# Kernel optimization log

Hardware: AMD Instinct MI355X
Metric: run time of the kernel (lower is better)

The kernel has to match this reference:

```python
import jax, jax.numpy as jnp
import numpy as np

NR, NL, K, TOPK, C, B = 4096, 16384, 8, 10, 16, 4
W_OCC, W_MDN, W_INT = 0.2, 1.0, 0.1
LOG2PI = float(np.log(2.0 * np.pi))


def setup_inputs() -> dict:
    key = jax.random.key(0)
    ks = jax.random.split(key, 12)
    radar_indices = jnp.concatenate([
        jax.random.randint(ks[0], (NR, 1), 0, B),
        jax.random.randint(ks[1], (NR, 1), 0, 41),
        jax.random.randint(ks[2], (NR, 2), 0, 176),
    ], axis=1).astype(jnp.int32)
    lidar_indices = jnp.concatenate([
        jax.random.randint(ks[3], (NL, 1), 0, B),
        jax.random.randint(ks[4], (NL, 1), 0, 41),
        jax.random.randint(ks[5], (NL, 2), 0, 176),
    ], axis=1).astype(jnp.int32)
    return {
        'mu_off': jax.random.normal(ks[6], (NR, K, 3)) * 2.0,
        'log_sig_off': jax.random.normal(ks[7], (NR, K, 3)) * 0.3,
        'mu_int': jax.random.normal(ks[8], (NR, K, 1)),
        'occ_logit': jax.random.normal(ks[9], (NR, K, 1)),
        'mix_logit': jax.random.normal(ks[10], (NR, K, 1)),
        'lidar_features': jax.random.normal(ks[11], (NL, C)),
        'radar_indices': radar_indices,
        'lidar_indices': lidar_indices,
        'gt_topk': TOPK,
    }


def _match(radar_indices, lidar_indices, topk):
    # per-batch top-k nearest lidar voxels for each radar voxel (vectorized:
    # dense masked distance matrix replaces the per-batch python loop)
    rb, lb = radar_indices[:, 0], lidar_indices[:, 0]
    rpos = radar_indices[:, 1:].astype(jnp.float32)  # (Nr,3) zyx
    lpos = lidar_indices[:, 1:].astype(jnp.float32)  # (Nl,3)
    d2 = ((rpos * rpos).sum(-1)[:, None] + (lpos * lpos).sum(-1)[None, :]
          - 2.0 * (rpos @ lpos.T))  # (Nr,Nl) squared dist, same order as cdist
    same = rb[:, None] == lb[None, :]
    d2 = jnp.where(same, d2, jnp.inf)  # cross-batch pairs excluded
    _, nn_idx = jax.lax.top_k(-d2, topk)  # (Nr,topk) smallest distances
    matched = same.any(axis=1)  # (Nr,)
    offs_zyx = (lidar_indices[nn_idx, 1:]
                - radar_indices[:, None, 1:]).astype(jnp.float32)  # (Nr,topk,3)
    offs_zyx = jnp.where(matched[:, None, None], offs_zyx, 0.0)
    return matched, nn_idx, offs_zyx


def reference(mu_off, log_sig_off, mu_int, occ_logit, mix_logit,
              lidar_features, radar_indices, lidar_indices, gt_topk):
    matched, nn_idx, offs_zyx = _match(radar_indices, lidar_indices, gt_topk)
    gt_feat = jnp.where(matched[:, None, None], lidar_features[nn_idx], 0.0)  # (Nr,T,C)
    y = offs_zyx[..., ::-1]  # flip zyx -> xyz, (Nr,T,3)

    # occupancy BCE-with-logits against matched mask
    occ_any = occ_logit[..., 0].max(axis=1)  # (Nr,)
    tgt = matched.astype(occ_any.dtype)
    occ_loss = (tgt * jax.nn.softplus(-occ_any)
                + (1.0 - tgt) * jax.nn.softplus(occ_any)).mean()

    # MDN log-prob: (Nr,T,K) mixture components
    log_pi = jax.nn.log_softmax(mix_logit[..., 0], axis=1)  # (Nr,K)
    mu_ = mu_off[:, None, :, :]       # (Nr,1,K,3)
    ls_ = log_sig_off[:, None, :, :]
    sigma2 = jnp.exp(2.0 * ls_) + 1e-12
    y_ = y[:, :, None, :]             # (Nr,T,1,3)
    logN = -0.5 * (((y_ - mu_) ** 2) / sigma2 + 2.0 * ls_ + LOG2PI).sum(-1)  # (Nr,T,K)
    log_post = logN + log_pi[:, None, :]
    logp = jax.nn.logsumexp(log_post, axis=-1)  # (Nr,T)

    # masked means emulate boolean-index-then-mean over matched rows
    m = matched.astype(jnp.float32)
    cnt = m.sum()
    T = logp.shape[1]
    mdn_nll = -(logp * m[:, None]).sum() / (cnt * T)

    # intensity loss (C % 4 == 0 path)
    gt_int = gt_feat.reshape(gt_feat.shape[0], gt_feat.shape[1], C // 4, 4)[..., 3].mean(axis=2)  # (Nr,T)
    r = jax.nn.softmax(log_post, axis=-1)  # (Nr,T,K) responsibilities
    term = r * jnp.abs(mu_int[:, None, :, 0] - gt_int[:, :, None])  # (Nr,T,K)
    int_loss = (term * m[:, None, None]).sum() / (cnt * T * r.shape[-1])

    return W_OCC * occ_loss + W_MDN * mdn_nll + W_INT * int_loss
```

## Files before the change

kernel.cpp:

```cpp
#include <hip/hip_runtime.h>
#include <cstdint>

#define NRAD 4096
#define NLID 16384
#define KMIX 8
#define TOPK 10
#define CF   16
#define LOG2PI 1.8378770664093453f
#define MAIN_BLOCKS 1024

static constexpr unsigned INF_D2 = 62851u;

__device__ __forceinline__ void insert_key(unsigned (&t)[TOPK], unsigned key) {
#pragma unroll
    for (int i = TOPK - 1; i >= 1; --i) {
        unsigned hi = key > t[i - 1] ? key : t[i - 1];
        t[i] = hi < t[i] ? hi : t[i];
    }
    t[0] = key < t[0] ? key : t[0];
}

__device__ __forceinline__ void merge10(unsigned (&t)[TOPK], int lane,
                                        unsigned& mine, unsigned& first, unsigned& tenth) {
#pragma unroll
    for (int r = 0; r < TOPK; ++r) {
        unsigned v = t[0];
#pragma unroll
        for (int off = 32; off >= 1; off >>= 1) {
            unsigned o = __shfl_xor(v, off, 64);
            v = o < v ? o : v;
        }
        if (t[0] == v) {
#pragma unroll
            for (int i = 0; i < TOPK - 1; ++i) t[i] = t[i + 1];
            t[TOPK - 1] = 0xFFFFFFFFu;
        }
        if (lane == r) mine = v;
        if (r == 0) first = v;
        if (r == TOPK - 1) tenth = v;
    }
}

__device__ __forceinline__ float waveReduceSum(float v) {
#pragma unroll
    for (int off = 32; off >= 1; off >>= 1) v += __shfl_down(v, off, 64);
    return v;
}

__global__ __launch_bounds__(256) void prep_kernel(
        const int* __restrict__ lidar_indices,
        unsigned* __restrict__ packed_full,
        uint2* __restrict__ compacted,
        int* __restrict__ cursor) {
    int i = blockIdx.x * 256 + threadIdx.x;
    int lane = threadIdx.x & 63;
    int4 li = ((const int4*)lidar_indices)[i];
    int b = li.x;
    unsigned pos = ((unsigned)li.y << 16) | ((unsigned)li.z << 8) | (unsigned)li.w;
    packed_full[i] = ((unsigned)b << 22) | pos;
#pragma unroll
    for (int b2 = 0; b2 < 4; ++b2) {
        unsigned long long mask = __ballot(b == b2);
        if (b == b2) {
            int leader = __ffsll(mask) - 1;
            int off = (int)__popcll(mask & ((1ull << lane) - 1ull));
            int s = 0;
            if (lane == leader) s = atomicAdd(&cursor[b2], (int)__popcll(mask));
            s = __shfl(s, leader, 64);
            compacted[b2 * NLID + s + off] = make_uint2(pos, (unsigned)i);
        }
    }
}

__global__ __launch_bounds__(256) void main_kernel(
        const float* __restrict__ mu_off, const float* __restrict__ log_sig_off,
        const float* __restrict__ mu_int, const float* __restrict__ occ_logit,
        const float* __restrict__ mix_logit, const float* __restrict__ lidar_features,
        const int* __restrict__ radar_indices, const int* __restrict__ lidar_indices,
        const uint2* __restrict__ compacted, const unsigned* __restrict__ packed_full,
        const int* __restrict__ cursor, float4* __restrict__ partials,
        unsigned* __restrict__ dctr, float* __restrict__ out) {
    int tid = threadIdx.x, lane = tid & 63, wid = tid >> 6;
    int row = blockIdx.x * 4 + wid;

    int4 ri = ((const int4*)radar_indices)[row];
    int rb = ri.x, rz = ri.y, ry = ri.z, rx = ri.w;
    int c_cnt = cursor[rb];

    unsigned t[TOPK];
#pragma unroll
    for (int i = 0; i < TOPK; ++i) t[i] = 0xFFFFFFFFu;

    const uint4* src = (const uint4*)(compacted + rb * NLID);
    int iters = (c_cnt + 127) >> 7;
    uint4 q0 = src[lane];
    uint4 q1 = src[64 + lane];
    for (int it = 0; it < iters; ++it) {
        uint4 qn = src[(it + 2) * 64 + lane];
        int c0 = (it * 64 + lane) * 2;
        {
            int dz = (int)((q0.x >> 16) & 63u)  - rz;
            int dy = (int)((q0.x >> 8)  & 255u) - ry;
            int dx = (int)(q0.x & 255u)         - rx;
            unsigned d2 = (unsigned)(dz * dz + dy * dy + dx * dx);
            unsigned key = (c0 < c_cnt) ? ((d2 << 14) | q0.y) : 0xFFFFFFFFu;
            if (key < t[TOPK - 1]) insert_key(t, key);
        }
        {
            int dz = (int)((q0.z >> 16) & 63u)  - rz;
            int dy = (int)((q0.z >> 8)  & 255u) - ry;
            int dx = (int)(q0.z & 255u)         - rx;
            unsigned d2 = (unsigned)(dz * dz + dy * dy + dx * dx);
            unsigned key = (c0 + 1 < c_cnt) ? ((d2 << 14) | q0.w) : 0xFFFFFFFFu;
            if (key < t[TOPK - 1]) insert_key(t, key);
        }
        q0 = q1; q1 = qn;
    }

    unsigned mine = 0, first = 0, tenth = 0;
    merge10(t, lane, mine, first, tenth);
    bool matched = true;

    if (tenth == 0xFFFFFFFFu) {
#pragma unroll
        for (int i = 0; i < TOPK; ++i) t[i] = 0xFFFFFFFFu;
        for (int it = 0; it < NLID / 256; ++it) {
            uint4 p4 = ((const uint4*)packed_full)[it * 64 + lane];
            unsigned base = it * 256 + lane * 4;
            unsigned ps[4] = {p4.x, p4.y, p4.z, p4.w};
#pragma unroll
            for (int j = 0; j < 4; ++j) {
                unsigned p = ps[j];
                int b  = (int)(p >> 22);
                int dz = (int)((p >> 16) & 63u)  - rz;
                int dy = (int)((p >> 8)  & 255u) - ry;
                int dx = (int)(p & 255u)         - rx;
                unsigned d2 = (unsigned)(dz * dz + dy * dy + dx * dx);
                unsigned hi = (b == rb) ? d2 : INF_D2;
                insert_key(t, (hi << 14) | (base + j));
            }
        }
        merge10(t, lane, mine, first, tenth);
        matched = first < (INF_D2 << 14);
    }

    float mf = matched ? 1.f : 0.f;
    float lp = 0.f, ip = 0.f, oc = 0.f, mc = 0.f;
    if (lane < TOPK) {
        int nni = (int)(mine & 0x3FFFu);
        int4 ll = ((const int4*)lidar_indices)[nni];
        float y0 = mf * (float)(ll.w - rx);
        float y1 = mf * (float)(ll.z - ry);
        float y2 = mf * (float)(ll.y - rz);

        float mix[KMIX];
        float mmax = -1e30f;
#pragma unroll
        for (int k = 0; k < KMIX; ++k) {
            mix[k] = mix_logit[row * KMIX + k];
            mmax = fmaxf(mmax, mix[k]);
        }
        float msum = 0.f;
#pragma unroll
        for (int k = 0; k < KMIX; ++k) msum += __expf(mix[k] - mmax);
        float logZ = mmax + __logf(msum);

        float lpost[KMIX];
        float pmax = -1e30f;
#pragma unroll
        for (int k = 0; k < KMIX; ++k) {
            int bidx = (row * KMIX + k) * 3;
            float mu0 = mu_off[bidx + 0], mu1 = mu_off[bidx + 1], mu2 = mu_off[bidx + 2];
            float l0 = log_sig_off[bidx + 0], l1 = log_sig_off[bidx + 1], l2 = log_sig_off[bidx + 2];
            float s0 = __expf(2.f * l0) + 1e-12f;
            float s1 = __expf(2.f * l1) + 1e-12f;
            float s2 = __expf(2.f * l2) + 1e-12f;
            float d0 = y0 - mu0, d1 = y1 - mu1, d2v = y2 - mu2;
            float qq = d0 * d0 / s0 + d1 * d1 / s1 + d2v * d2v / s2
                     + 2.f * (l0 + l1 + l2) + 3.f * LOG2PI;
            lpost[k] = -0.5f * qq + (mix[k] - logZ);
            pmax = fmaxf(pmax, lpost[k]);
        }
        float ex[KMIX];
        float se = 0.f;
#pragma unroll
        for (int k = 0; k < KMIX; ++k) { ex[k] = __expf(lpost[k] - pmax); se += ex[k]; }
        float logp = pmax + __logf(se);

        float gt = 0.f;
        if (matched) {
            const float* lf = lidar_features + nni * CF;
            gt = 0.25f * (lf[3] + lf[7] + lf[11] + lf[15]);
        }
        float inv_se = 1.f / se;
        float isum = 0.f;
#pragma unroll
        for (int k = 0; k < KMIX; ++k)
            isum += ex[k] * inv_se * fabsf(mu_int[row * KMIX + k] - gt);

        lp = mf * logp;
        ip = mf * isum;
        if (lane == 0) {
            float oa = -1e30f;
#pragma unroll
            for (int k = 0; k < KMIX; ++k) oa = fmaxf(oa, occ_logit[row * KMIX + k]);
            float soft_abs = log1pf(__expf(-fabsf(oa)));
            oc = mf * (soft_abs + fmaxf(-oa, 0.f)) + (1.f - mf) * (soft_abs + fmaxf(oa, 0.f));
            mc = mf;
        }
    }

    lp = waveReduceSum(lp); ip = waveReduceSum(ip);
    oc = waveReduceSum(oc); mc = waveReduceSum(mc);
    __shared__ float sA[4], sB[4], sC[4], sD[4];
    __shared__ int isLast;
    if (lane == 0) { sA[wid] = lp; sB[wid] = ip; sC[wid] = oc; sD[wid] = mc; }
    __syncthreads();
    if (tid == 0) {
        partials[blockIdx.x] = make_float4(sA[0] + sA[1] + sA[2] + sA[3],
                                           sB[0] + sB[1] + sB[2] + sB[3],
                                           sC[0] + sC[1] + sC[2] + sC[3],
                                           sD[0] + sD[1] + sD[2] + sD[3]);
        __threadfence();
        unsigned done = atomicAdd(dctr, 1u);
        isLast = (done == (unsigned)(MAIN_BLOCKS - 1)) ? 1 : 0;
    }
    __syncthreads();
    if (isLast) {
        __threadfence();
        float a = 0.f, b = 0.f, c = 0.f, d = 0.f;
        for (int i = tid; i < MAIN_BLOCKS; i += 256) {
            float4 p = partials[i];
            a += p.x; b += p.y; c += p.z; d += p.w;
        }
        a = waveReduceSum(a); b = waveReduceSum(b);
        c = waveReduceSum(c); d = waveReduceSum(d);
        if (lane == 0) { sA[wid] = a; sB[wid] = b; sC[wid] = c; sD[wid] = d; }
        __syncthreads();
        if (tid == 0) {
            a = sA[0] + sA[1] + sA[2] + sA[3];
            b = sB[0] + sB[1] + sB[2] + sB[3];
            c = sC[0] + sC[1] + sC[2] + sC[3];
            d = sD[0] + sD[1] + sD[2] + sD[3];
            float occ_loss = c / (float)NRAD;
            float mdn_nll  = -a / (d * (float)TOPK);
            float int_loss = b / (d * (float)TOPK * (float)KMIX);
            out[0] = 0.2f * occ_loss + mdn_nll + 0.1f * int_loss;
        }
    }
}

extern "C" void kernel_launch(void* const* d_in, const int* in_sizes, int n_in,
                              void* d_out, int out_size, void* d_ws, size_t ws_size,
                              hipStream_t stream) {
    const float* mu_off         = (const float*)d_in[0];
    const float* log_sig_off    = (const float*)d_in[1];
    const float* mu_int         = (const float*)d_in[2];
    const float* occ_logit      = (const float*)d_in[3];
    const float* mix_logit      = (const float*)d_in[4];
    const float* lidar_features = (const float*)d_in[5];
    const int*   radar_indices  = (const int*)d_in[6];
    const int*   lidar_indices  = (const int*)d_in[7];
    float* out = (float*)d_out;

    char* ws = (char*)d_ws;
    unsigned* packed_full = (unsigned*)(ws + 0);
    uint2*    compacted   = (uint2*)(ws + 65536);
    int*      cursor      = (int*)(ws + 589824);
    unsigned* dctr        = (unsigned*)(ws + 589840);
    float4*   partials    = (float4*)(ws + 589888);

    hipMemsetAsync(ws + 589824, 0, 64, stream);

    hipLaunchKernelGGL(prep_kernel, dim3(NLID / 256), dim3(256), 0, stream,
                       lidar_indices, packed_full, compacted, cursor);
    hipLaunchKernelGGL(main_kernel, dim3(MAIN_BLOCKS), dim3(256), 0, stream,
                       mu_off, log_sig_off, mu_int, occ_logit, mix_logit,
                       lidar_features, radar_indices, lidar_indices,
                       compacted, packed_full, cursor, partials, dctr, out);
}
```

Baseline: 130.4 us.

## Split each radar row's lidar scan across two waves with radius prefilter

Each radar row is now handled by two wavefronts that scan alternating chunks of the batch-compacted lidar list, doubling the block count. The merged top-10 is built from both halves through shared memory and a wave-wide shuffle selection. A fixed squared-distance cutoff (225) skips insertion of far candidates, and if fewer than ten candidates survive, a full unfiltered rescan of the compacted list runs, followed by the original global fallback. This halves the per-wave serial scan length and cuts insertion work, at the cost of an extra sync and merge, half the waves idling during the loss computation, and a costly fallback for rows with few close neighbours.

```diff
diff --git a/kernel.cpp b/kernel.cpp
--- a/kernel.cpp
+++ b/kernel.cpp
@@ -7,7 +7,8 @@
 #define TOPK 10
 #define CF   16
 #define LOG2PI 1.8378770664093453f
-#define MAIN_BLOCKS 1024
+#define MAIN_BLOCKS 2048
+#define R2T 225u
 
 static constexpr unsigned INF_D2 = 62851u;
 
@@ -81,7 +82,8 @@
         const int* __restrict__ cursor, float4* __restrict__ partials,
         unsigned* __restrict__ dctr, float* __restrict__ out) {
     int tid = threadIdx.x, lane = tid & 63, wid = tid >> 6;
-    int row = blockIdx.x * 4 + wid;
+    int half = wid & 1;
+    int row  = blockIdx.x * 2 + (wid >> 1);
 
     int4 ri = ((const int4*)radar_indices)[row];
     int rb = ri.x, rz = ri.y, ry = ri.z, rx = ri.w;
@@ -93,120 +95,170 @@
 
     const uint4* src = (const uint4*)(compacted + rb * NLID);
     int iters = (c_cnt + 127) >> 7;
-    uint4 q0 = src[lane];
-    uint4 q1 = src[64 + lane];
-    for (int it = 0; it < iters; ++it) {
+    uint4 q = src[half * 64 + lane];
+    for (int it = half; it < iters; it += 2) {
         uint4 qn = src[(it + 2) * 64 + lane];
         int c0 = (it * 64 + lane) * 2;
         {
-            int dz = (int)((q0.x >> 16) & 63u)  - rz;
-            int dy = (int)((q0.x >> 8)  & 255u) - ry;
-            int dx = (int)(q0.x & 255u)         - rx;
+            int dz = (int)((q.x >> 16) & 63u)  - rz;
+            int dy = (int)((q.x >> 8)  & 255u) - ry;
+            int dx = (int)(q.x & 255u)         - rx;
             unsigned d2 = (unsigned)(dz * dz + dy * dy + dx * dx);
-            unsigned key = (c0 < c_cnt) ? ((d2 << 14) | q0.y) : 0xFFFFFFFFu;
-            if (key < t[TOPK - 1]) insert_key(t, key);
+            if (d2 <= R2T && c0 < c_cnt) insert_key(t, (d2 << 14) | q.y);
         }
         {
-            int dz = (int)((q0.z >> 16) & 63u)  - rz;
-            int dy = (int)((q0.z >> 8)  & 255u) - ry;
-            int dx = (int)(q0.z & 255u)         - rx;
+            int dz = (int)((q.z >> 16) & 63u)  - rz;
+            int dy = (int)((q.z >> 8)  & 255u) - ry;
+            int dx = (int)(q.z & 255u)         - rx;
             unsigned d2 = (unsigned)(dz * dz + dy * dy + dx * dx);
-            unsigned key = (c0 + 1 < c_cnt) ? ((d2 << 14) | q0.w) : 0xFFFFFFFFu;
-            if (key < t[TOPK - 1]) insert_key(t, key);
-        }
-        q0 = q1; q1 = qn;
+            if (d2 <= R2T && c0 + 1 < c_cnt) insert_key(t, (d2 << 14) | q.w);
+        }
+        q = qn;
     }
 
     unsigned mine = 0, first = 0, tenth = 0;
     merge10(t, lane, mine, first, tenth);
-    bool matched = true;
-
-    if (tenth == 0xFFFFFFFFu) {
-#pragma unroll
-        for (int i = 0; i < TOPK; ++i) t[i] = 0xFFFFFFFFu;
-        for (int it = 0; it < NLID / 256; ++it) {
-            uint4 p4 = ((const uint4*)packed_full)[it * 64 + lane];
-            unsigned base = it * 256 + lane * 4;
-            unsigned ps[4] = {p4.x, p4.y, p4.z, p4.w};
-#pragma unroll
-            for (int j = 0; j < 4; ++j) {
-                unsigned p = ps[j];
-                int b  = (int)(p >> 22);
-                int dz = (int)((p >> 16) & 63u)  - rz;
-                int dy = (int)((p >> 8)  & 255u) - ry;
-                int dx = (int)(p & 255u)         - rx;
-                unsigned d2 = (unsigned)(dz * dz + dy * dy + dx * dx);
-                unsigned hi = (b == rb) ? d2 : INF_D2;
-                insert_key(t, (hi << 14) | (base + j));
-            }
-        }
-        merge10(t, lane, mine, first, tenth);
-        matched = first < (INF_D2 << 14);
-    }
-
-    float mf = matched ? 1.f : 0.f;
+
+    __shared__ unsigned pairbuf[4][16];
+    if (lane < TOPK) pairbuf[wid][lane] = mine;
+    __syncthreads();
+
     float lp = 0.f, ip = 0.f, oc = 0.f, mc = 0.f;
-    if (lane < TOPK) {
-        int nni = (int)(mine & 0x3FFFu);
-        int4 ll = ((const int4*)lidar_indices)[nni];
-        float y0 = mf * (float)(ll.w - rx);
-        float y1 = mf * (float)(ll.z - ry);
-        float y2 = mf * (float)(ll.y - rz);
-
-        float mix[KMIX];
-        float mmax = -1e30f;
-#pragma unroll
-        for (int k = 0; k < KMIX; ++k) {
-            mix[k] = mix_logit[row * KMIX + k];
-            mmax = fmaxf(mmax, mix[k]);
-        }
-        float msum = 0.f;
-#pragma unroll
-        for (int k = 0; k < KMIX; ++k) msum += __expf(mix[k] - mmax);
-        float logZ = mmax + __logf(msum);
-
-        float lpost[KMIX];
-        float pmax = -1e30f;
-#pragma unroll
-        for (int k = 0; k < KMIX; ++k) {
-            int bidx = (row * KMIX + k) * 3;
-            float mu0 = mu_off[bidx + 0], mu1 = mu_off[bidx + 1], mu2 = mu_off[bidx + 2];
-            float l0 = log_sig_off[bidx + 0], l1 = log_sig_off[bidx + 1], l2 = log_sig_off[bidx + 2];
-            float s0 = __expf(2.f * l0) + 1e-12f;
-            float s1 = __expf(2.f * l1) + 1e-12f;
-            float s2 = __expf(2.f * l2) + 1e-12f;
-            float d0 = y0 - mu0, d1 = y1 - mu1, d2v = y2 - mu2;
-            float qq = d0 * d0 / s0 + d1 * d1 / s1 + d2v * d2v / s2
-                     + 2.f * (l0 + l1 + l2) + 3.f * LOG2PI;
-            lpost[k] = -0.5f * qq + (mix[k] - logZ);
-            pmax = fmaxf(pmax, lpost[k]);
-        }
-        float ex[KMIX];
-        float se = 0.f;
-#pragma unroll
-        for (int k = 0; k < KMIX; ++k) { ex[k] = __expf(lpost[k] - pmax); se += ex[k]; }
-        float logp = pmax + __logf(se);
-
-        float gt = 0.f;
-        if (matched) {
-            const float* lf = lidar_features + nni * CF;
-            gt = 0.25f * (lf[3] + lf[7] + lf[11] + lf[15]);
-        }
-        float inv_se = 1.f / se;
-        float isum = 0.f;
-#pragma unroll
-        for (int k = 0; k < KMIX; ++k)
-            isum += ex[k] * inv_se * fabsf(mu_int[row * KMIX + k] - gt);
-
-        lp = mf * logp;
-        ip = mf * isum;
-        if (lane == 0) {
-            float oa = -1e30f;
-#pragma unroll
-            for (int k = 0; k < KMIX; ++k) oa = fmaxf(oa, occ_logit[row * KMIX + k]);
-            float soft_abs = log1pf(__expf(-fabsf(oa)));
-            oc = mf * (soft_abs + fmaxf(-oa, 0.f)) + (1.f - mf) * (soft_abs + fmaxf(oa, 0.f));
-            mc = mf;
+    if (half == 0) {
+        unsigned k = 0xFFFFFFFFu;
+        if (lane < TOPK)           k = pairbuf[wid][lane];
+        else if (lane < 2 * TOPK)  k = pairbuf[wid + 1][lane - TOPK];
+        unsigned fin = 0xFFFFFFFFu;
+        first = 0xFFFFFFFFu; tenth = 0xFFFFFFFFu;
+#pragma unroll
+        for (int r = 0; r < TOPK; ++r) {
+            unsigned v = k;
+#pragma unroll
+            for (int off = 32; off >= 1; off >>= 1) {
+                unsigned o = __shfl_xor(v, off, 64);
+                v = o < v ? o : v;
+            }
+            if (k == v) k = 0xFFFFFFFFu;
+            if (lane == r) fin = v;
+            if (r == 0) first = v;
+            if (r == TOPK - 1) tenth = v;
+        }
+        bool matched = true;
+
+        if (tenth == 0xFFFFFFFFu) {
+#pragma unroll
+            for (int i = 0; i < TOPK; ++i) t[i] = 0xFFFFFFFFu;
+            uint4 q0 = src[lane];
+            for (int it = 0; it < iters; ++it) {
+                uint4 qn2 = src[(it + 1) * 64 + lane];
+                int c0 = (it * 64 + lane) * 2;
+                {
+                    int dz = (int)((q0.x >> 16) & 63u)  - rz;
+                    int dy = (int)((q0.x >> 8)  & 255u) - ry;
+                    int dx = (int)(q0.x & 255u)         - rx;
+                    unsigned d2 = (unsigned)(dz * dz + dy * dy + dx * dx);
+                    unsigned key = (c0 < c_cnt) ? ((d2 << 14) | q0.y) : 0xFFFFFFFFu;
+                    insert_key(t, key);
+                }
+                {
+                    int dz = (int)((q0.z >> 16) & 63u)  - rz;
+                    int dy = (int)((q0.z >> 8)  & 255u) - ry;
+                    int dx = (int)(q0.z & 255u)         - rx;
+                    unsigned d2 = (unsigned)(dz * dz + dy * dy + dx * dx);
+                    unsigned key = (c0 + 1 < c_cnt) ? ((d2 << 14) | q0.w) : 0xFFFFFFFFu;
+                    insert_key(t, key);
+                }
+                q0 = qn2;
+            }
+            merge10(t, lane, fin, first, tenth);
+
+            if (tenth == 0xFFFFFFFFu) {
+#pragma unroll
+                for (int i = 0; i < TOPK; ++i) t[i] = 0xFFFFFFFFu;
+                for (int it = 0; it < NLID / 256; ++it) {
+                    uint4 p4 = ((const uint4*)packed_full)[it * 64 + lane];
+                    unsigned base = it * 256 + lane * 4;
+                    unsigned ps[4] = {p4.x, p4.y, p4.z, p4.w};
+#pragma unroll
+                    for (int j = 0; j < 4; ++j) {
+                        unsigned p = ps[j];
+                        int b  = (int)(p >> 22);
+                        int dz = (int)((p >> 16) & 63u)  - rz;
+                        int dy = (int)((p >> 8)  & 255u) - ry;
+                        int dx = (int)(p & 255u)         - rx;
+                        unsigned d2 = (unsigned)(dz * dz + dy * dy + dx * dx);
+                        unsigned hi = (b == rb) ? d2 : INF_D2;
+                        insert_key(t, (hi << 14) | (base + j));
+                    }
+                }
+                merge10(t, lane, fin, first, tenth);
+                matched = first < (INF_D2 << 14);
+            }
+        }
+
+        float mf = matched ? 1.f : 0.f;
+        if (lane < TOPK) {
+            int nni = (int)(fin & 0x3FFFu);
+            int4 ll = ((const int4*)lidar_indices)[nni];
+            float y0 = mf * (float)(ll.w - rx);
+            float y1 = mf * (float)(ll.z - ry);
+            float y2 = mf * (float)(ll.y - rz);
+
+            float mix[KMIX];
+            float mmax = -1e30f;
+#pragma unroll
+            for (int kk = 0; kk < KMIX; ++kk) {
+                mix[kk] = mix_logit[row * KMIX + kk];
+                mmax = fmaxf(mmax, mix[kk]);
+            }
+            float msum = 0.f;
+#pragma unroll
+            for (int kk = 0; kk < KMIX; ++kk) msum += __expf(mix[kk] - mmax);
+            float logZ = mmax + __logf(msum);
+
+            float lpost[KMIX];
+            float pmax = -1e30f;
+#pragma unroll
+            for (int kk = 0; kk < KMIX; ++kk) {
+                int bidx = (row * KMIX + kk) * 3;
+                float mu0 = mu_off[bidx + 0], mu1 = mu_off[bidx + 1], mu2 = mu_off[bidx + 2];
+                float l0 = log_sig_off[bidx + 0], l1 = log_sig_off[bidx + 1], l2 = log_sig_off[bidx + 2];
+                float s0 = __expf(2.f * l0) + 1e-12f;
+                float s1 = __expf(2.f * l1) + 1e-12f;
+                float s2 = __expf(2.f * l2) + 1e-12f;
+                float d0 = y0 - mu0, d1 = y1 - mu1, d2v = y2 - mu2;
+                float qq = d0 * d0 / s0 + d1 * d1 / s1 + d2v * d2v / s2
+                         + 2.f * (l0 + l1 + l2) + 3.f * LOG2PI;
+                lpost[kk] = -0.5f * qq + (mix[kk] - logZ);
+                pmax = fmaxf(pmax, lpost[kk]);
+            }
+            float ex[KMIX];
+            float se = 0.f;
+#pragma unroll
+            for (int kk = 0; kk < KMIX; ++kk) { ex[kk] = __expf(lpost[kk] - pmax); se += ex[kk]; }
+            float logp = pmax + __logf(se);
+
+            float gt = 0.f;
+            if (matched) {
+                const float* lf = lidar_features + nni * CF;
+                gt = 0.25f * (lf[3] + lf[7] + lf[11] + lf[15]);
+            }
+            float inv_se = 1.f / se;
+            float isum = 0.f;
+#pragma unroll
+            for (int kk = 0; kk < KMIX; ++kk)
+                isum += ex[kk] * inv_se * fabsf(mu_int[row * KMIX + kk] - gt);
+
+            lp = mf * logp;
+            ip = mf * isum;
+            if (lane == 0) {
+                float oa = -1e30f;
+#pragma unroll
+                for (int kk = 0; kk < KMIX; ++kk) oa = fmaxf(oa, occ_logit[row * KMIX + kk]);
+                float soft_abs = log1pf(__expf(-fabsf(oa)));
+                oc = mf * (soft_abs + fmaxf(-oa, 0.f)) + (1.f - mf) * (soft_abs + fmaxf(oa, 0.f));
+                mc = mf;
+            }
         }
     }
 
```

Result: slower. 177.6 us (+36.1%).

## Bin lidar voxels into a coarse spatial grid for the radius-limited kNN search

Applied to the files above, without the earlier changes.

The prep kernel now scatters each lidar voxel into a fixed-capacity bucket of a per-batch 3x11x11 grid of 16-voxel cells. The main kernel searches only the 27 neighbouring cells, with the lanes of a wave spread across x-cells and slots. It keeps candidates within radius 15 and falls back to the old per-batch compacted scan, then to the full scan, when a cell overflows or fewer than ten neighbours are found. This replaces the linear scan over about 4096 same-batch points per radar row with a few hundred gathered loads, but adds per-voxel atomics in prep and a fallback path that may fire often when cell occupancy exceeds the capacity of 21.

```diff
diff --git a/kernel.cpp b/kernel.cpp
--- a/kernel.cpp
+++ b/kernel.cpp
@@ -8,6 +8,9 @@
 #define CF   16
 #define LOG2PI 1.8378770664093453f
 #define MAIN_BLOCKS 1024
+#define NCELL 363
+#define CAP   21
+#define R2T   225u
 
 static constexpr unsigned INF_D2 = 62851u;
 
@@ -51,6 +54,8 @@
         const int* __restrict__ lidar_indices,
         unsigned* __restrict__ packed_full,
         uint2* __restrict__ compacted,
+        uint2* __restrict__ cells,
+        int* __restrict__ cellcnt,
         int* __restrict__ cursor) {
     int i = blockIdx.x * 256 + threadIdx.x;
     int lane = threadIdx.x & 63;
@@ -58,6 +63,11 @@
     int b = li.x;
     unsigned pos = ((unsigned)li.y << 16) | ((unsigned)li.z << 8) | (unsigned)li.w;
     packed_full[i] = ((unsigned)b << 22) | pos;
+
+    int g = b * NCELL + (li.y >> 4) * 121 + (li.z >> 4) * 11 + (li.w >> 4);
+    int slot = atomicAdd(&cellcnt[g], 1);
+    if (slot < CAP) cells[g * CAP + slot] = make_uint2(pos, (unsigned)i);
+
 #pragma unroll
     for (int b2 = 0; b2 < 4; ++b2) {
         unsigned long long mask = __ballot(b == b2);
@@ -78,6 +88,7 @@
         const float* __restrict__ mix_logit, const float* __restrict__ lidar_features,
         const int* __restrict__ radar_indices, const int* __restrict__ lidar_indices,
         const uint2* __restrict__ compacted, const unsigned* __restrict__ packed_full,
+        const uint2* __restrict__ cells, const int* __restrict__ cellcnt,
         const int* __restrict__ cursor, float4* __restrict__ partials,
         unsigned* __restrict__ dctr, float* __restrict__ out) {
     int tid = threadIdx.x, lane = tid & 63, wid = tid >> 6;
@@ -85,63 +96,93 @@
 
     int4 ri = ((const int4*)radar_indices)[row];
     int rb = ri.x, rz = ri.y, ry = ri.z, rx = ri.w;
-    int c_cnt = cursor[rb];
+    int cz = rz >> 4, cy = ry >> 4, cx = rx >> 4;
 
     unsigned t[TOPK];
 #pragma unroll
     for (int i = 0; i < TOPK; ++i) t[i] = 0xFFFFFFFFu;
 
-    const uint4* src = (const uint4*)(compacted + rb * NLID);
-    int iters = (c_cnt + 127) >> 7;
-    uint4 q0 = src[lane];
-    uint4 q1 = src[64 + lane];
-    for (int it = 0; it < iters; ++it) {
-        uint4 qn = src[(it + 2) * 64 + lane];
-        int c0 = (it * 64 + lane) * 2;
-        {
-            int dz = (int)((q0.x >> 16) & 63u)  - rz;
-            int dy = (int)((q0.x >> 8)  & 255u) - ry;
-            int dx = (int)(q0.x & 255u)         - rx;
-            unsigned d2 = (unsigned)(dz * dz + dy * dy + dx * dx);
-            unsigned key = (c0 < c_cnt) ? ((d2 << 14) | q0.y) : 0xFFFFFFFFu;
-            if (key < t[TOPK - 1]) insert_key(t, key);
-        }
-        {
-            int dz = (int)((q0.z >> 16) & 63u)  - rz;
-            int dy = (int)((q0.z >> 8)  & 255u) - ry;
-            int dx = (int)(q0.z & 255u)         - rx;
-            unsigned d2 = (unsigned)(dz * dz + dy * dy + dx * dx);
-            unsigned key = (c0 + 1 < c_cnt) ? ((d2 << 14) | q0.w) : 0xFFFFFFFFu;
-            if (key < t[TOPK - 1]) insert_key(t, key);
-        }
-        q0 = q1; q1 = qn;
+    int j    = lane / CAP;
+    int slot = lane - j * CAP;
+    int xc   = cx - 1 + j;
+    bool lane_ok = (lane < 63) && ((unsigned)xc <= 10u);
+    bool needs_fb = false;
+
+#pragma unroll
+    for (int dzy = 0; dzy < 9; ++dzy) {
+        int zc = cz + (dzy / 3) - 1;
+        int yc = cy + (dzy % 3) - 1;
+        bool cellok = lane_ok && ((unsigned)zc <= 2u) && ((unsigned)yc <= 10u);
+        int g = rb * NCELL + zc * 121 + yc * 11 + xc;
+        int n = cellcnt[g];
+        uint2 c = cells[g * CAP + slot];
+        needs_fb |= cellok && (n > CAP);
+        bool active = cellok && (slot < n);
+        int dz = (int)((c.x >> 16) & 63u)  - rz;
+        int dy = (int)((c.x >> 8)  & 255u) - ry;
+        int dx = (int)(c.x & 255u)         - rx;
+        unsigned d2 = (unsigned)(dz * dz + dy * dy + dx * dx);
+        if (active && d2 <= R2T) insert_key(t, (d2 << 14) | c.y);
     }
 
     unsigned mine = 0, first = 0, tenth = 0;
     merge10(t, lane, mine, first, tenth);
     bool matched = true;
-
-    if (tenth == 0xFFFFFFFFu) {
+    bool fb = (__ballot(needs_fb) != 0ull) || (tenth == 0xFFFFFFFFu);
+
+    if (fb) {
+        int c_cnt = cursor[rb];
+        const uint4* src = (const uint4*)(compacted + rb * NLID);
+        int iters = (c_cnt + 127) >> 7;
 #pragma unroll
         for (int i = 0; i < TOPK; ++i) t[i] = 0xFFFFFFFFu;
-        for (int it = 0; it < NLID / 256; ++it) {
-            uint4 p4 = ((const uint4*)packed_full)[it * 64 + lane];
-            unsigned base = it * 256 + lane * 4;
-            unsigned ps[4] = {p4.x, p4.y, p4.z, p4.w};
-#pragma unroll
-            for (int j = 0; j < 4; ++j) {
-                unsigned p = ps[j];
-                int b  = (int)(p >> 22);
-                int dz = (int)((p >> 16) & 63u)  - rz;
-                int dy = (int)((p >> 8)  & 255u) - ry;
-                int dx = (int)(p & 255u)         - rx;
+        uint4 q0 = src[lane];
+        uint4 q1 = src[64 + lane];
+        for (int it = 0; it < iters; ++it) {
+            uint4 qn = src[(it + 2) * 64 + lane];
+            int c0 = (it * 64 + lane) * 2;
+            {
+                int dz = (int)((q0.x >> 16) & 63u)  - rz;
+                int dy = (int)((q0.x >> 8)  & 255u) - ry;
+                int dx = (int)(q0.x & 255u)         - rx;
                 unsigned d2 = (unsigned)(dz * dz + dy * dy + dx * dx);
-                unsigned hi = (b == rb) ? d2 : INF_D2;
-                insert_key(t, (hi << 14) | (base + j));
+                unsigned key = (c0 < c_cnt) ? ((d2 << 14) | q0.y) : 0xFFFFFFFFu;
+                if (key < t[TOPK - 1]) insert_key(t, key);
             }
+            {
+                int dz = (int)((q0.z >> 16) & 63u)  - rz;
+                int dy = (int)((q0.z >> 8)  & 255u) - ry;
+                int dx = (int)(q0.z & 255u)         - rx;
+                unsigned d2 = (unsigned)(dz * dz + dy * dy + dx * dx);
+                unsigned key = (c0 + 1 < c_cnt) ? ((d2 << 14) | q0.w) : 0xFFFFFFFFu;
+                if (key < t[TOPK - 1]) insert_key(t, key);
+            }
+            q0 = q1; q1 = qn;
         }
         merge10(t, lane, mine, first, tenth);
-        matched = first < (INF_D2 << 14);
+
+        if (tenth == 0xFFFFFFFFu) {
+#pragma unroll
+            for (int i = 0; i < TOPK; ++i) t[i] = 0xFFFFFFFFu;
+            for (int it = 0; it < NLID / 256; ++it) {
+                uint4 p4 = ((const uint4*)packed_full)[it * 64 + lane];
+                unsigned base = it * 256 + lane * 4;
+                unsigned ps[4] = {p4.x, p4.y, p4.z, p4.w};
+#pragma unroll
+                for (int jj = 0; jj < 4; ++jj) {
+                    unsigned p = ps[jj];
+                    int b  = (int)(p >> 22);
+                    int dz = (int)((p >> 16) & 63u)  - rz;
+                    int dy = (int)((p >> 8)  & 255u) - ry;
+                    int dx = (int)(p & 255u)         - rx;
+                    unsigned d2 = (unsigned)(dz * dz + dy * dy + dx * dx);
+                    unsigned hi = (b == rb) ? d2 : INF_D2;
+                    insert_key(t, (hi << 14) | (base + jj));
+                }
+            }
+            merge10(t, lane, mine, first, tenth);
+            matched = first < (INF_D2 << 14);
+        }
     }
 
     float mf = matched ? 1.f : 0.f;
@@ -266,16 +307,19 @@
     char* ws = (char*)d_ws;
     unsigned* packed_full = (unsigned*)(ws + 0);
     uint2*    compacted   = (uint2*)(ws + 65536);
-    int*      cursor      = (int*)(ws + 589824);
-    unsigned* dctr        = (unsigned*)(ws + 589840);
-    float4*   partials    = (float4*)(ws + 589888);
-
-    hipMemsetAsync(ws + 589824, 0, 64, stream);
+    uint2*    cells       = (uint2*)(ws + 589824);
+    int*      cellcnt     = (int*)(ws + 834560);
+    int*      cursor      = (int*)(ws + 840368);
+    unsigned* dctr        = (unsigned*)(ws + 840384);
+    float4*   partials    = (float4*)(ws + 840448);
+
+    hipMemsetAsync(ws + 834560, 0, 5888, stream);
 
     hipLaunchKernelGGL(prep_kernel, dim3(NLID / 256), dim3(256), 0, stream,
-                       lidar_indices, packed_full, compacted, cursor);
+                       lidar_indices, packed_full, compacted, cells, cellcnt, cursor);
     hipLaunchKernelGGL(main_kernel, dim3(MAIN_BLOCKS), dim3(256), 0, stream,
                        mu_off, log_sig_off, mu_int, occ_logit, mix_logit,
                        lidar_features, radar_indices, lidar_indices,
-                       compacted, packed_full, cursor, partials, dctr, out);
-}
+                       compacted, packed_full, cells, cellcnt, cursor,
+                       partials, dctr, out);
+}
```

After: 131.1 us. About the same (+0.6%).
